# Kernel optimization log

Measured on AMD Instinct MI355X. Metric: run time of the kernel, lower is better.

Reference implementation:

```python
import jax, jax.numpy as jnp
import numpy as np

B, T, D = 2, 1024, 1024
H, HKV = 16, 8
HD = D // H           # 64
NREP = H // HKV       # 2
NLAYERS = 3
MAXKV = T * NLAYERS   # 3072
EPS = 1e-5


def setup_inputs() -> dict:
    key = jax.random.key(0)
    ks = jax.random.split(key, 8)
    # rotary tables over full accumulated-KV range
    inv_freq = 1.0 / (10000.0 ** (jnp.arange(0, HD, 2, dtype=jnp.float32) / HD))  # (HD/2,)
    t = jnp.arange(MAXKV, dtype=jnp.float32)
    freqs = jnp.outer(t, inv_freq)  # (MAXKV, HD/2)
    return {
        "x": jax.random.normal(ks[0], (B, T, D), jnp.float32),
        "cos": jnp.cos(freqs),
        "sin": jnp.sin(freqs),
        "q_w": jax.random.normal(ks[1], (NLAYERS, D, D), jnp.float32) * 0.02,
        "k_w": jax.random.normal(ks[2], (NLAYERS, D // NREP, D), jnp.float32) * 0.02,
        "v_w": jax.random.normal(ks[3], (NLAYERS, D // NREP, D), jnp.float32) * 0.02,
        "ln_w": jnp.ones((NLAYERS, D), jnp.float32),
        "lam": jax.random.normal(ks[4], (NLAYERS,), jnp.float32) * 0.1,
        "out_w": jax.random.normal(ks[5], (D, D), jnp.float32) * 0.02,
        "final_ln_w": jnp.ones((D,), jnp.float32),
        "alpha": jnp.ones((1,), jnp.float32),
    }


def rmsnorm(x, w):
    return x * jax.lax.rsqrt(jnp.mean(x * x, axis=-1, keepdims=True) + EPS) * w


def rope(x, cos, sin):
    # x: (B, L, h, HD); cos/sin: (MAXKV, HD/2); flash_attn non-interleaved rotary
    L = x.shape[1]
    c = jnp.concatenate([cos[:L], cos[:L]], axis=-1)[None, :, None, :]
    s = jnp.concatenate([sin[:L], sin[:L]], axis=-1)[None, :, None, :]
    x1, x2 = jnp.split(x, 2, axis=-1)
    rot = jnp.concatenate([-x2, x1], axis=-1)
    return x * c + rot * s


def reference(x, cos, sin, q_w, k_w, v_w, ln_w, lam, out_w, final_ln_w, alpha):
    scale = HD ** -0.5
    # lambda weights: layernorm over sigmoid of the 3 scalars (biased var, eps=1e-5)
    s = jax.nn.sigmoid(lam)
    lw = (s - s.mean()) * jax.lax.rsqrt(s.var() + EPS)
    qidx = jnp.arange(T)
    k_list, v_list = [], []
    acc = jnp.zeros_like(x)
    for i in range(NLAYERS):
        q = (x @ q_w[i].T).reshape(B, T, H, HD)
        k = (x @ k_w[i].T).reshape(B, T, HKV, HD)
        v = (x @ v_w[i].T).reshape(B, T, HKV, HD)
        k_list.append(k)
        v_list.append(v)
        K = jnp.concatenate(k_list, axis=1)  # (B, L, HKV, HD), L=(i+1)*T
        V = jnp.concatenate(v_list, axis=1)
        L = K.shape[1]
        qr = rope(q, cos, sin)
        Kr = rope(K, cos, sin)  # whole buffer re-rotated each layer, as in original
        Kr = jnp.repeat(Kr, NREP, axis=2)  # GQA expand
        Vr = jnp.repeat(V, NREP, axis=2)
        scores = jnp.einsum('bqhd,bkhd->bhqk', qr, Kr) * scale
        # flash_attn causal=True with kv_len > q_len aligns bottom-right
        mask = jnp.arange(L)[None, :] <= (qidx + (L - T))[:, None]
        scores = jnp.where(mask[None, None], scores, -jnp.inf)
        attn = jax.nn.softmax(scores, axis=-1)
        o = jnp.einsum('bhqk,bkhd->bqhd', attn, Vr).reshape(B, T, D)
        acc = acc + rmsnorm(o, ln_w[i]) * lw[i]
    out = rmsnorm(acc + alpha * x, final_ln_w)
    return out @ out_w.T
```

## Files before the change

kernel.cpp:

```cpp
#include <hip/hip_runtime.h>
#include <type_traits>
#include <utility>

typedef unsigned short u16;
typedef unsigned int u32;
typedef short short8 __attribute__((ext_vector_type(8)));
typedef __bf16 bf16x8 __attribute__((ext_vector_type(8)));
typedef float floatx4 __attribute__((ext_vector_type(4)));

template <typename V, typename = void> struct MfmaTakes : std::false_type {};
template <typename V>
struct MfmaTakes<V, std::void_t<decltype(__builtin_amdgcn_mfma_f32_16x16x32_bf16(
    std::declval<V>(), std::declval<V>(), std::declval<floatx4>(), 0, 0, 0))>>
    : std::true_type {};

template <typename V>
__device__ __forceinline__ floatx4 mfma_impl(V a, V b, floatx4 c, std::true_type) {
  return __builtin_amdgcn_mfma_f32_16x16x32_bf16(a, b, c, 0, 0, 0);
}
template <typename V>
__device__ __forceinline__ floatx4 mfma_impl(V a, V b, floatx4 c, std::false_type) {
  return __builtin_amdgcn_mfma_f32_16x16x32_bf16(
      __builtin_bit_cast(bf16x8, a), __builtin_bit_cast(bf16x8, b), c, 0, 0, 0);
}
__device__ __forceinline__ floatx4 MFMA16(short8 a, short8 b, floatx4 c) {
  return mfma_impl<short8>(a, b, c, MfmaTakes<short8>{});
}

__device__ __forceinline__ u16 f2bf(float f) {
  union { float f; unsigned u; } x; x.f = f;
  unsigned r = (x.u + 0x7fffu + ((x.u >> 16) & 1u)) >> 16;
  return (u16)r;
}
__device__ __forceinline__ float bf2f(u16 v) {
  union { unsigned u; float f; } x; x.u = ((unsigned)v) << 16; return x.f;
}
__device__ __forceinline__ u32 packbf(float lo, float hi) {
  return (__float_as_uint(hi) & 0xffff0000u) | (__float_as_uint(lo) >> 16);
}
__device__ __forceinline__ u32 pack2bf(float lo, float hi) {
  return ((u32)f2bf(hi) << 16) | (u32)f2bf(lo);
}

#if defined(__has_builtin)
#if __has_builtin(__builtin_amdgcn_global_load_lds)
#define HAS_GLLDS 1
#endif
#endif
__device__ __forceinline__ void stage16(const u16* g, u16* lbase, int lane) {
#ifdef HAS_GLLDS
  __builtin_amdgcn_global_load_lds(
      (__attribute__((address_space(1))) void*)(g),
      (__attribute__((address_space(3))) void*)(lbase), 16, 0, 0);
#else
  *(uint4*)(lbase + lane * 8) = *(const uint4*)g;
#endif
}

__global__ __launch_bounds__(256) void prep_kernel(
    const float* __restrict__ x, const float* __restrict__ qw,
    const float* __restrict__ kw, const float* __restrict__ vw,
    const float* __restrict__ outw, const float* __restrict__ lam,
    u16* __restrict__ xb, u16* __restrict__ wcat, u16* __restrict__ outwb,
    float* __restrict__ lwbuf) {
  size_t gid = (size_t)blockIdx.x * 256 + threadIdx.x;
  if (gid == 0) {
    float s0 = 1.f / (1.f + expf(-lam[0]));
    float s1 = 1.f / (1.f + expf(-lam[1]));
    float s2 = 1.f / (1.f + expf(-lam[2]));
    float mean = (s0 + s1 + s2) * (1.f / 3.f);
    float d0 = s0 - mean, d1 = s1 - mean, d2 = s2 - mean;
    float var = (d0 * d0 + d1 * d1 + d2 * d2) * (1.f / 3.f);
    float r = rsqrtf(var + 1e-5f);
    lwbuf[0] = d0 * r; lwbuf[1] = d1 * r; lwbuf[2] = d2 * r;
  }
  if (gid < 524288) {
    float4 v = ((const float4*)x)[gid];
    ushort4 o; o.x = f2bf(v.x); o.y = f2bf(v.y); o.z = f2bf(v.z); o.w = f2bf(v.w);
    ((ushort4*)xb)[gid] = o;
    return;
  }
  size_t g2 = gid - 524288;
  if (g2 < 1572864) {
    int col4 = (int)(g2 & 255);
    int n = (int)(g2 >> 8);
    int layer = n >> 11, r = n & 2047;
    const float* srcrow;
    if (r < 1024) srcrow = qw + ((size_t)(layer * 1024 + r) << 10);
    else if (r < 1536) srcrow = kw + ((size_t)(layer * 512 + (r - 1024)) << 10);
    else srcrow = vw + ((size_t)(layer * 512 + (r - 1536)) << 10);
    float4 v = ((const float4*)srcrow)[col4];
    ushort4 o; o.x = f2bf(v.x); o.y = f2bf(v.y); o.z = f2bf(v.z); o.w = f2bf(v.w);
    ((ushort4*)wcat)[g2] = o;
    return;
  }
  size_t g3 = g2 - 1572864;
  if (g3 < 262144) {
    float4 v = ((const float4*)outw)[g3];
    ushort4 o; o.x = f2bf(v.x); o.y = f2bf(v.y); o.z = f2bf(v.z); o.w = f2bf(v.w);
    ((ushort4*)outwb)[g3] = o;
  }
}

__global__ __launch_bounds__(256) void gemm_qkv(
    const u16* __restrict__ A, const u16* __restrict__ Bw,
    const float* __restrict__ cosb, const float* __restrict__ sinb,
    u16* __restrict__ qr, u16* __restrict__ kr, u16* __restrict__ vt) {
  __shared__ u16 As[128][64];
  __shared__ u16 Bs[128][64];
  const unsigned flat = blockIdx.x;
  const int bm = (flat >> 3) & 15;
  const int bn = ((flat >> 7) << 3) + (flat & 7);
  const int tid = threadIdx.x;
  const int wave = tid >> 6, lane = tid & 63;
  const int quad = lane >> 4, l16 = lane & 15;
  const int wm = wave & 1, wn = wave >> 1;
  const int srow = lane >> 3, skc = (lane & 7) * 8;
  floatx4 acc[4][4];
#pragma unroll
  for (int i = 0; i < 4; i++)
#pragma unroll
    for (int j = 0; j < 4; j++) { acc[i][j][0] = 0.f; acc[i][j][1] = 0.f; acc[i][j][2] = 0.f; acc[i][j][3] = 0.f; }
  const u16* Abase = A + (size_t)(bm * 128) * 1024;
  const u16* Bbase = Bw + (size_t)(bn * 128) * 1024;
  for (int k0 = 0; k0 < 1024; k0 += 64) {
    __syncthreads();
#pragma unroll
    for (int i = 0; i < 4; i++) {
      int ch = wave * 4 + i;
      stage16(Abase + (size_t)(ch * 8 + srow) * 1024 + k0 + skc, &As[ch * 8][0], lane);
      stage16(Bbase + (size_t)(ch * 8 + srow) * 1024 + k0 + skc, &Bs[ch * 8][0], lane);
    }
    __syncthreads();
#pragma unroll
    for (int kf = 0; kf < 2; kf++) {
      short8 af[4], bf[4];
#pragma unroll
      for (int mi = 0; mi < 4; mi++)
        af[mi] = *(const short8*)(&As[wm * 64 + mi * 16 + l16][kf * 32 + quad * 8]);
#pragma unroll
      for (int ni = 0; ni < 4; ni++)
        bf[ni] = *(const short8*)(&Bs[wn * 64 + ni * 16 + l16][kf * 32 + quad * 8]);
#pragma unroll
      for (int mi = 0; mi < 4; mi++)
#pragma unroll
        for (int ni = 0; ni < 4; ni++)
          acc[mi][ni] = MFMA16(af[mi], bf[ni], acc[mi][ni]);
    }
  }
  const int f0 = bn * 128 + wn * 64;
  const int lay = f0 >> 11;
  const int r0 = f0 & 2047;
  const int mrow0 = bm * 128 + wm * 64;
  if (r0 < 1024) {
    const int h = r0 >> 6;
#pragma unroll
    for (int mi = 0; mi < 4; mi++)
#pragma unroll
      for (int rr = 0; rr < 4; rr++) {
        int m = mrow0 + mi * 16 + quad * 4 + rr;
        int b = m >> 10, t = m & 1023;
        const float* cp = cosb + (size_t)t * 32;
        const float* sp = sinb + (size_t)t * 32;
        float c0 = cp[l16], s0 = sp[l16];
        float c1 = cp[16 + l16], s1 = sp[16 + l16];
        float x10 = acc[mi][0][rr], x20 = acc[mi][2][rr];
        float x11 = acc[mi][1][rr], x21 = acc[mi][3][rr];
        u16* row = qr + ((((size_t)lay * 2 + b) * 16 + h) * 1024 + t) * 64;
        row[l16]      = f2bf((x10 * c0 - x20 * s0) * 0.125f);
        row[16 + l16] = f2bf((x11 * c1 - x21 * s1) * 0.125f);
        row[32 + l16] = f2bf((x20 * c0 + x10 * s0) * 0.125f);
        row[48 + l16] = f2bf((x21 * c1 + x11 * s1) * 0.125f);
      }
  } else if (r0 < 1536) {
    const int hk = (r0 - 1024) >> 6;
#pragma unroll
    for (int mi = 0; mi < 4; mi++)
#pragma unroll
      for (int rr = 0; rr < 4; rr++) {
        int m = mrow0 + mi * 16 + quad * 4 + rr;
        int b = m >> 10, t = m & 1023;
        int pos = lay * 1024 + t;
        const float* cp = cosb + (size_t)pos * 32;
        const float* sp = sinb + (size_t)pos * 32;
        float c0 = cp[l16], s0 = sp[l16];
        float c1 = cp[16 + l16], s1 = sp[16 + l16];
        float x10 = acc[mi][0][rr], x20 = acc[mi][2][rr];
        float x11 = acc[mi][1][rr], x21 = acc[mi][3][rr];
        u16* row = kr + (((size_t)(b * 8 + hk)) * 3072 + pos) * 64;
        row[l16]      = f2bf(x10 * c0 - x20 * s0);
        row[16 + l16] = f2bf(x11 * c1 - x21 * s1);
        row[32 + l16] = f2bf(x20 * c0 + x10 * s0);
        row[48 + l16] = f2bf(x21 * c1 + x11 * s1);
      }
  } else {
    const int hv = (r0 - 1536) >> 6;
#pragma unroll
    for (int mi = 0; mi < 4; mi++) {
      int m0 = mrow0 + mi * 16 + quad * 4;
      int b = m0 >> 10;
      int pos0 = lay * 1024 + (m0 & 1023);
      u16* colbase = vt + ((size_t)(b * 8 + hv) * 64) * 3072 + pos0;
#pragma unroll
      for (int ni = 0; ni < 4; ni++) {
        int d = ni * 16 + l16;
        uint2 st;
        st.x = pack2bf(acc[mi][ni][0], acc[mi][ni][1]);
        st.y = pack2bf(acc[mi][ni][2], acc[mi][ni][3]);
        *(uint2*)(colbase + (size_t)d * 3072) = st;
      }
    }
  }
}

__global__ __launch_bounds__(256) void gemm_bt(
    const u16* __restrict__ A, const u16* __restrict__ Bw,
    float* __restrict__ C, int N, int K) {
  __shared__ u16 As[64][72];
  __shared__ u16 Bs[64][72];
  const int bm = blockIdx.x, bn = blockIdx.y;
  const int tid = threadIdx.x;
  const int wave = tid >> 6, lane = tid & 63;
  const int quad = lane >> 4, l16 = lane & 15;
  const int lr = tid >> 2, lc = (tid & 3) << 4;
  floatx4 acc[4];
#pragma unroll
  for (int i = 0; i < 4; i++) { acc[i][0] = 0.f; acc[i][1] = 0.f; acc[i][2] = 0.f; acc[i][3] = 0.f; }
  const u16* Arow = A + (size_t)(bm * 64 + lr) * K;
  const u16* Brow = Bw + (size_t)(bn * 64 + lr) * K;
  for (int k0 = 0; k0 < K; k0 += 64) {
    __syncthreads();
    *(uint4*)(&As[lr][lc])     = *(const uint4*)(Arow + k0 + lc);
    *(uint4*)(&As[lr][lc + 8]) = *(const uint4*)(Arow + k0 + lc + 8);
    *(uint4*)(&Bs[lr][lc])     = *(const uint4*)(Brow + k0 + lc);
    *(uint4*)(&Bs[lr][lc + 8]) = *(const uint4*)(Brow + k0 + lc + 8);
    __syncthreads();
    const int mrow = wave * 16 + l16;
    short8 a0 = *(const short8*)(&As[mrow][quad * 8]);
    short8 a1 = *(const short8*)(&As[mrow][32 + quad * 8]);
#pragma unroll
    for (int ns = 0; ns < 4; ns++) {
      short8 b0 = *(const short8*)(&Bs[ns * 16 + l16][quad * 8]);
      short8 b1 = *(const short8*)(&Bs[ns * 16 + l16][32 + quad * 8]);
      acc[ns] = MFMA16(a0, b0, acc[ns]);
      acc[ns] = MFMA16(a1, b1, acc[ns]);
    }
  }
#pragma unroll
  for (int ns = 0; ns < 4; ns++)
#pragma unroll
    for (int r = 0; r < 4; r++) {
      int row = bm * 64 + wave * 16 + quad * 4 + r;
      int col = bn * 64 + ns * 16 + l16;
      C[(size_t)row * N + col] = acc[ns][r];
    }
}

__global__ __launch_bounds__(256) void attn_v5(
    const u16* __restrict__ qr, const u16* __restrict__ kr,
    const u16* __restrict__ vt, u16* __restrict__ obS,
    float* __restrict__ lbufp) {
  __shared__ u16 Kt[32][72];
  __shared__ u16 Vtt[64][40];
  __shared__ u16 Pw[4][16][40];
  const unsigned flat = blockIdx.x;
  const int bhz = (int)((flat >> 6) * 8 + (flat & 7));
  const int qtile = 7 - (int)((flat >> 3) & 7);
  const int z = bhz >> 5;
  const int bh = bhz & 31;
  const int lay = (z == 5) ? 0 : ((z == 0 || z == 4) ? 1 : 2);
  const int n = lay * 32 + qtile * 4 + 4;
  int kt0, kt1;
  if (lay == 0) { kt0 = 0; kt1 = n; }
  else if (lay == 1) { int hf = n >> 1; kt0 = (z == 0) ? 0 : hf; kt1 = (z == 0) ? hf : n; }
  else {
    int t1 = n / 3, t2 = (2 * n) / 3;
    kt0 = (z == 1) ? 0 : ((z == 2) ? t1 : t2);
    kt1 = (z == 1) ? t1 : ((z == 2) ? t2 : n);
  }
  const int maskkt = lay * 32 + qtile * 4;
  const int b = bh >> 4, h = bh & 15, hk = h >> 1;
  const int tid = threadIdx.x, wave = tid >> 6, lane = tid & 63;
  const int quad = lane >> 4, l16 = lane & 15;
  const int qeffbase = lay * 1024 + qtile * 128 + wave * 32;
  const u16* qpb = qr + ((((size_t)lay * 2 + b) * 16 + h) * 1024
                         + qtile * 128 + wave * 32 + l16) * 64 + quad * 8;
  short8 qf[2][2];
  qf[0][0] = *(const short8*)(qpb);
  qf[0][1] = *(const short8*)(qpb + 32);
  qf[1][0] = *(const short8*)(qpb + 1024);
  qf[1][1] = *(const short8*)(qpb + 1056);
  const short8 ones = {16256, 16256, 16256, 16256, 16256, 16256, 16256, 16256};
  floatx4 oacc[2][4];
#pragma unroll
  for (int nt = 0; nt < 2; nt++)
#pragma unroll
    for (int dt = 0; dt < 4; dt++) { oacc[nt][dt][0] = 0.f; oacc[nt][dt][1] = 0.f; oacc[nt][dt][2] = 0.f; oacc[nt][dt][3] = 0.f; }
  floatx4 lacc[2];
  lacc[0][0] = 0.f; lacc[0][1] = 0.f; lacc[0][2] = 0.f; lacc[0][3] = 0.f;
  lacc[1] = lacc[0];
  const int ksr = tid >> 3, ksc = (tid & 7) * 8;
  const int vdr = tid >> 2, vdc = (tid & 3) * 8;
  const u16* kp = kr + ((size_t)(b * 8 + hk) * 3072 + kt0 * 32 + ksr) * 64 + ksc;
  const u16* vp = vt + ((size_t)(b * 8 + hk) * 64 + vdr) * 3072 + kt0 * 32 + vdc;
  uint4 kA = *(const uint4*)kp;
  uint4 vA = *(const uint4*)vp;
  for (int kt = kt0; kt < kt1; kt++) {
    kp += 2048; vp += 32;
    __syncthreads();
    *(uint4*)(&Kt[ksr][ksc])  = kA;
    *(uint4*)(&Vtt[vdr][vdc]) = vA;
    if (kt + 1 < kt1) { kA = *(const uint4*)kp; vA = *(const uint4*)vp; }
    __syncthreads();
    const bool needmask = (kt >= maskkt);
    uint2 pk[2][2];
#pragma unroll
    for (int mt = 0; mt < 2; mt++) {
      short8 kfa = *(const short8*)(&Kt[mt * 16 + l16][quad * 8]);
      short8 kfb = *(const short8*)(&Kt[mt * 16 + l16][32 + quad * 8]);
      const int keyb = kt * 32 + mt * 16 + quad * 4;
#pragma unroll
      for (int nt = 0; nt < 2; nt++) {
        floatx4 s; s[0] = 0.f; s[1] = 0.f; s[2] = 0.f; s[3] = 0.f;
        s = MFMA16(kfa, qf[nt][0], s);
        s = MFMA16(kfb, qf[nt][1], s);
        float p0 = __expf(s[0]), p1 = __expf(s[1]);
        float p2 = __expf(s[2]), p3 = __expf(s[3]);
        if (needmask) {
          int qpos = qeffbase + nt * 16 + l16;
          if (keyb + 0 > qpos) p0 = 0.f;
          if (keyb + 1 > qpos) p1 = 0.f;
          if (keyb + 2 > qpos) p2 = 0.f;
          if (keyb + 3 > qpos) p3 = 0.f;
        }
        pk[mt][nt].x = packbf(p0, p1);
        pk[mt][nt].y = packbf(p2, p3);
      }
    }
    short8 vf[4];
#pragma unroll
    for (int dt = 0; dt < 4; dt++)
      vf[dt] = *(const short8*)(&Vtt[dt * 16 + l16][quad * 8]);
#pragma unroll
    for (int nt = 0; nt < 2; nt++) {
      *(uint2*)(&Pw[wave][l16][quad * 4])      = pk[0][nt];
      *(uint2*)(&Pw[wave][l16][16 + quad * 4]) = pk[1][nt];
      short8 pf = *(const short8*)(&Pw[wave][l16][quad * 8]);
      lacc[nt] = MFMA16(ones, pf, lacc[nt]);
#pragma unroll
      for (int dt = 0; dt < 4; dt++)
        oacc[nt][dt] = MFMA16(vf[dt], pf, oacc[nt][dt]);
    }
  }
  float* Pf = (float*)(&Pw[wave][0][0]);
  const int tt = lane >> 2, dd = (lane & 3) << 2;
#pragma unroll
  for (int nt = 0; nt < 2; nt++) {
    int t = qtile * 128 + wave * 32 + nt * 16 + l16;
    if (quad == 0)
      lbufp[((size_t)z * 2048 + b * 1024 + t) * 16 + h] = lacc[nt][0];
    int t2 = qtile * 128 + wave * 32 + nt * 16 + tt;
    u16* orow = obS + ((size_t)(z * 2 + b) * 1024 + t2) * 1024 + h * 64 + dd;
#pragma unroll
    for (int dt = 0; dt < 4; dt++) {
      *(floatx4*)(&Pf[l16 * 20 + quad * 4]) = oacc[nt][dt];
      floatx4 val = *(const floatx4*)(&Pf[tt * 20 + dd]);
      uint2 st; st.x = pack2bf(val[0], val[1]); st.y = pack2bf(val[2], val[3]);
      *(uint2*)(orow + dt * 16) = st;
    }
  }
}

__device__ __forceinline__ float block_sum(float v, float* red) {
  v += __shfl_xor(v, 32); v += __shfl_xor(v, 16); v += __shfl_xor(v, 8);
  v += __shfl_xor(v, 4);  v += __shfl_xor(v, 2);  v += __shfl_xor(v, 1);
  __syncthreads();
  if ((threadIdx.x & 63) == 0) red[threadIdx.x >> 6] = v;
  __syncthreads();
  return red[0] + red[1] + red[2] + red[3];
}

__global__ __launch_bounds__(256) void fused_norm(
    const u16* __restrict__ obS, const float* __restrict__ lbufp,
    const float* __restrict__ x, const float* __restrict__ lnw,
    const float* __restrict__ lwbuf, const float* __restrict__ flnw,
    const float* __restrict__ alphap, u16* __restrict__ y) {
  __shared__ float red[4];
  const int row = blockIdx.x, tid = threadIdx.x;
  float a[4] = {0.f, 0.f, 0.f, 0.f};
  const int nsl[3] = {1, 2, 3};
  const int sl[3][3] = {{5, 0, 0}, {0, 4, 0}, {1, 2, 3}};
#pragma unroll
  for (int l = 0; l < 3; l++) {
    float o0 = 0.f, o1 = 0.f, o2 = 0.f, o3 = 0.f, ls = 0.f;
#pragma unroll
    for (int si = 0; si < 3; si++) {
      if (si >= nsl[l]) break;
      int z = sl[l][si];
      uint2 v = ((const uint2*)(obS + ((size_t)z * 2048 + row) * 1024))[tid];
      o0 += bf2f((u16)(v.x & 0xffff)); o1 += bf2f((u16)(v.x >> 16));
      o2 += bf2f((u16)(v.y & 0xffff)); o3 += bf2f((u16)(v.y >> 16));
      ls += lbufp[((size_t)z * 2048 + row) * 16 + (tid >> 4)];
    }
    float linv = 1.f / ls;
    float v0 = o0 * linv, v1 = o1 * linv, v2 = o2 * linv, v3 = o3 * linv;
    float ss = v0 * v0 + v1 * v1 + v2 * v2 + v3 * v3;
    ss = block_sum(ss, red);
    float rstd = rsqrtf(ss * (1.f / 1024.f) + 1e-5f);
    float lw = lwbuf[l];
    float4 w = ((const float4*)(lnw + (size_t)l * 1024))[tid];
    a[0] += v0 * rstd * w.x * lw;
    a[1] += v1 * rstd * w.y * lw;
    a[2] += v2 * rstd * w.z * lw;
    a[3] += v3 * rstd * w.w * lw;
  }
  const float aa = alphap[0];
  float4 xv = ((const float4*)(x + (size_t)row * 1024))[tid];
  float v0 = a[0] + aa * xv.x, v1 = a[1] + aa * xv.y;
  float v2 = a[2] + aa * xv.z, v3 = a[3] + aa * xv.w;
  float ss = v0 * v0 + v1 * v1 + v2 * v2 + v3 * v3;
  ss = block_sum(ss, red);
  float rstd = rsqrtf(ss * (1.f / 1024.f) + 1e-5f);
  float4 fw = ((const float4*)flnw)[tid];
  ushort4 o;
  o.x = f2bf(v0 * rstd * fw.x); o.y = f2bf(v1 * rstd * fw.y);
  o.z = f2bf(v2 * rstd * fw.z); o.w = f2bf(v3 * rstd * fw.w);
  ((ushort4*)(y + (size_t)row * 1024))[tid] = o;
}

extern "C" void kernel_launch(void* const* d_in, const int* in_sizes, int n_in,
                              void* d_out, int out_size, void* d_ws, size_t ws_size,
                              hipStream_t stream) {
  const float* x     = (const float*)d_in[0];
  const float* cosb  = (const float*)d_in[1];
  const float* sinb  = (const float*)d_in[2];
  const float* qw    = (const float*)d_in[3];
  const float* kw    = (const float*)d_in[4];
  const float* vw    = (const float*)d_in[5];
  const float* lnw   = (const float*)d_in[6];
  const float* lam   = (const float*)d_in[7];
  const float* outw  = (const float*)d_in[8];
  const float* flnw  = (const float*)d_in[9];
  const float* alphap= (const float*)d_in[10];
  float* out = (float*)d_out;
  char* ws = (char*)d_ws;
  u16*   xb    = (u16*)  (ws + 0);
  u16*   wcat  = (u16*)  (ws + 4194304);
  u16*   obS   = (u16*)  (ws + 0);
  u16*   outwb = (u16*)  (ws + 25165824);
  float* lwbuf = (float*)(ws + 27262976);
  u16*   qr    = (u16*)  (ws + 27264000);
  u16*   kr    = (u16*)  (ws + 39846912);
  u16*   vt    = (u16*)  (ws + 46138368);
  float* lbufp = (float*)(ws + 52429824);
  u16*   yb    = (u16*)  (ws + 53216256);

  prep_kernel<<<9216, 256, 0, stream>>>(x, qw, kw, vw, outw, lam, xb, wcat, outwb, lwbuf);
  gemm_qkv<<<768, 256, 0, stream>>>(xb, wcat, cosb, sinb, qr, kr, vt);
  attn_v5<<<1536, 256, 0, stream>>>(qr, kr, vt, obS, lbufp);
  fused_norm<<<2048, 256, 0, stream>>>(obS, lbufp, x, lnw, lwbuf, flnw, alphap, yb);
  gemm_bt<<<dim3(32, 16), 256, 0, stream>>>(yb, outwb, out, 1024, 1024);
}
```

Before: 252.0 us.

## Stage QKV epilogue through LDS for coalesced stores; load V fragments directly

The QKV GEMM epilogue now writes rotated Q/K and transposed V tiles into a per-wave LDS scratch area (reusing As) and then emits 16-byte coalesced global stores, replacing scattered 2-byte and 8-byte writes. The attention kernel drops the shared V tile and instead has each lane load its MFMA V fragments straight from global memory, software-pipelined one key tile ahead. This removes LDS traffic and shared-memory footprint for V, but each wave now fetches V redundantly and keeps more registers live.

```diff
diff --git a/kernel.cpp b/kernel.cpp
--- a/kernel.cpp
+++ b/kernel.cpp
@@ -148,66 +148,69 @@
           acc[mi][ni] = MFMA16(af[mi], bf[ni], acc[mi][ni]);
     }
   }
+  __syncthreads();
+  u16* Tw = (&As[0][0]) + (unsigned)wave * 1056;
   const int f0 = bn * 128 + wn * 64;
   const int lay = f0 >> 11;
   const int r0 = f0 & 2047;
   const int mrow0 = bm * 128 + wm * 64;
-  if (r0 < 1024) {
-    const int h = r0 >> 6;
-#pragma unroll
-    for (int mi = 0; mi < 4; mi++)
+  const int jrd = lane & 7, trd = lane >> 3;
+  if (r0 < 1536) {
+    const bool isQ = (r0 < 1024);
+    const int h = isQ ? (r0 >> 6) : ((r0 - 1024) >> 6);
+    const float qscale = isQ ? 0.125f : 1.f;
+    const int posoff = isQ ? 0 : lay * 1024;
+#pragma unroll
+    for (int mi = 0; mi < 4; mi++) {
 #pragma unroll
       for (int rr = 0; rr < 4; rr++) {
         int m = mrow0 + mi * 16 + quad * 4 + rr;
-        int b = m >> 10, t = m & 1023;
-        const float* cp = cosb + (size_t)t * 32;
-        const float* sp = sinb + (size_t)t * 32;
-        float c0 = cp[l16], s0 = sp[l16];
-        float c1 = cp[16 + l16], s1 = sp[16 + l16];
-        float x10 = acc[mi][0][rr], x20 = acc[mi][2][rr];
-        float x11 = acc[mi][1][rr], x21 = acc[mi][3][rr];
-        u16* row = qr + ((((size_t)lay * 2 + b) * 16 + h) * 1024 + t) * 64;
-        row[l16]      = f2bf((x10 * c0 - x20 * s0) * 0.125f);
-        row[16 + l16] = f2bf((x11 * c1 - x21 * s1) * 0.125f);
-        row[32 + l16] = f2bf((x20 * c0 + x10 * s0) * 0.125f);
-        row[48 + l16] = f2bf((x21 * c1 + x11 * s1) * 0.125f);
-      }
-  } else if (r0 < 1536) {
-    const int hk = (r0 - 1024) >> 6;
-#pragma unroll
-    for (int mi = 0; mi < 4; mi++)
-#pragma unroll
-      for (int rr = 0; rr < 4; rr++) {
-        int m = mrow0 + mi * 16 + quad * 4 + rr;
-        int b = m >> 10, t = m & 1023;
-        int pos = lay * 1024 + t;
+        int t = m & 1023;
+        int pos = posoff + t;
         const float* cp = cosb + (size_t)pos * 32;
         const float* sp = sinb + (size_t)pos * 32;
         float c0 = cp[l16], s0 = sp[l16];
         float c1 = cp[16 + l16], s1 = sp[16 + l16];
         float x10 = acc[mi][0][rr], x20 = acc[mi][2][rr];
         float x11 = acc[mi][1][rr], x21 = acc[mi][3][rr];
-        u16* row = kr + (((size_t)(b * 8 + hk)) * 3072 + pos) * 64;
-        row[l16]      = f2bf(x10 * c0 - x20 * s0);
-        row[16 + l16] = f2bf(x11 * c1 - x21 * s1);
-        row[32 + l16] = f2bf(x20 * c0 + x10 * s0);
-        row[48 + l16] = f2bf(x21 * c1 + x11 * s1);
+        u16* trow = Tw + (quad * 4 + rr) * 66;
+        trow[l16]      = f2bf((x10 * c0 - x20 * s0) * qscale);
+        trow[16 + l16] = f2bf((x11 * c1 - x21 * s1) * qscale);
+        trow[32 + l16] = f2bf((x20 * c0 + x10 * s0) * qscale);
+        trow[48 + l16] = f2bf((x21 * c1 + x11 * s1) * qscale);
       }
+#pragma unroll
+      for (int half = 0; half < 2; half++) {
+        int tloc = trd + half * 8;
+        uint4 val = *(const uint4*)(Tw + tloc * 66 + jrd * 8);
+        int m = mrow0 + mi * 16 + tloc;
+        int b = m >> 10, t = m & 1023;
+        u16* dst;
+        if (isQ) dst = qr + ((((size_t)lay * 2 + b) * 16 + h) * 1024 + t) * 64;
+        else     dst = kr + (((size_t)(b * 8 + h)) * 3072 + lay * 1024 + t) * 64;
+        *(uint4*)(dst + jrd * 8) = val;
+      }
+    }
   } else {
     const int hv = (r0 - 1536) >> 6;
-#pragma unroll
-    for (int mi = 0; mi < 4; mi++) {
-      int m0 = mrow0 + mi * 16 + quad * 4;
-      int b = m0 >> 10;
-      int pos0 = lay * 1024 + (m0 & 1023);
-      u16* colbase = vt + ((size_t)(b * 8 + hv) * 64) * 3072 + pos0;
-#pragma unroll
-      for (int ni = 0; ni < 4; ni++) {
-        int d = ni * 16 + l16;
-        uint2 st;
-        st.x = pack2bf(acc[mi][ni][0], acc[mi][ni][1]);
-        st.y = pack2bf(acc[mi][ni][2], acc[mi][ni][3]);
-        *(uint2*)(colbase + (size_t)d * 3072) = st;
+    const int b = mrow0 >> 10;
+    const int posb = lay * 1024 + (mrow0 & 1023);
+#pragma unroll
+    for (int ni = 0; ni < 4; ni++) {
+#pragma unroll
+      for (int mi = 0; mi < 4; mi++) {
+        u16* trow = Tw + l16 * 66 + mi * 16 + quad * 4;
+        trow[0] = f2bf(acc[mi][ni][0]);
+        trow[1] = f2bf(acc[mi][ni][1]);
+        trow[2] = f2bf(acc[mi][ni][2]);
+        trow[3] = f2bf(acc[mi][ni][3]);
+      }
+#pragma unroll
+      for (int half = 0; half < 2; half++) {
+        int dloc = trd + half * 8;
+        uint4 val = *(const uint4*)(Tw + dloc * 66 + jrd * 8);
+        u16* dst = vt + ((size_t)(b * 8 + hv) * 64 + ni * 16 + dloc) * 3072 + posb + jrd * 8;
+        *(uint4*)dst = val;
       }
     }
   }
@@ -256,12 +259,11 @@
     }
 }
 
-__global__ __launch_bounds__(256) void attn_v5(
+__global__ __launch_bounds__(256) void attn_v6(
     const u16* __restrict__ qr, const u16* __restrict__ kr,
     const u16* __restrict__ vt, u16* __restrict__ obS,
     float* __restrict__ lbufp) {
   __shared__ u16 Kt[32][72];
-  __shared__ u16 Vtt[64][40];
   __shared__ u16 Pw[4][16][40];
   const unsigned flat = blockIdx.x;
   const int bhz = (int)((flat >> 6) * 8 + (flat & 7));
@@ -300,17 +302,25 @@
   lacc[0][0] = 0.f; lacc[0][1] = 0.f; lacc[0][2] = 0.f; lacc[0][3] = 0.f;
   lacc[1] = lacc[0];
   const int ksr = tid >> 3, ksc = (tid & 7) * 8;
-  const int vdr = tid >> 2, vdc = (tid & 3) * 8;
   const u16* kp = kr + ((size_t)(b * 8 + hk) * 3072 + kt0 * 32 + ksr) * 64 + ksc;
-  const u16* vp = vt + ((size_t)(b * 8 + hk) * 64 + vdr) * 3072 + kt0 * 32 + vdc;
+  const u16* vwb = vt + (size_t)(b * 8 + hk) * 64 * 3072 + (size_t)l16 * 3072 + quad * 8;
   uint4 kA = *(const uint4*)kp;
-  uint4 vA = *(const uint4*)vp;
+  short8 vf[4], vfN[4];
+#pragma unroll
+  for (int dt = 0; dt < 4; dt++)
+    vfN[dt] = *(const short8*)(vwb + (size_t)(dt * 16) * 3072 + kt0 * 32);
   for (int kt = kt0; kt < kt1; kt++) {
-    kp += 2048; vp += 32;
-    __syncthreads();
-    *(uint4*)(&Kt[ksr][ksc])  = kA;
-    *(uint4*)(&Vtt[vdr][vdc]) = vA;
-    if (kt + 1 < kt1) { kA = *(const uint4*)kp; vA = *(const uint4*)vp; }
+    kp += 2048;
+    __syncthreads();
+    *(uint4*)(&Kt[ksr][ksc]) = kA;
+    if (kt + 1 < kt1) kA = *(const uint4*)kp;
+#pragma unroll
+    for (int dt = 0; dt < 4; dt++) vf[dt] = vfN[dt];
+    if (kt + 1 < kt1) {
+#pragma unroll
+      for (int dt = 0; dt < 4; dt++)
+        vfN[dt] = *(const short8*)(vwb + (size_t)(dt * 16) * 3072 + (kt + 1) * 32);
+    }
     __syncthreads();
     const bool needmask = (kt >= maskkt);
     uint2 pk[2][2];
@@ -337,10 +347,6 @@
         pk[mt][nt].y = packbf(p2, p3);
       }
     }
-    short8 vf[4];
-#pragma unroll
-    for (int dt = 0; dt < 4; dt++)
-      vf[dt] = *(const short8*)(&Vtt[dt * 16 + l16][quad * 8]);
 #pragma unroll
     for (int nt = 0; nt < 2; nt++) {
       *(uint2*)(&Pw[wave][l16][quad * 4])      = pk[0][nt];
@@ -457,7 +463,7 @@
 
   prep_kernel<<<9216, 256, 0, stream>>>(x, qw, kw, vw, outw, lam, xb, wcat, outwb, lwbuf);
   gemm_qkv<<<768, 256, 0, stream>>>(xb, wcat, cosb, sinb, qr, kr, vt);
-  attn_v5<<<1536, 256, 0, stream>>>(qr, kr, vt, obS, lbufp);
+  attn_v6<<<1536, 256, 0, stream>>>(qr, kr, vt, obS, lbufp);
   fused_norm<<<2048, 256, 0, stream>>>(obS, lbufp, x, lnw, lwbuf, flnw, alphap, yb);
   gemm_bt<<<dim3(32, 16), 256, 0, stream>>>(yb, outwb, out, 1024, 1024);
 }
```

After: 282.0 us. 11.9% more time.

## Process two KV tiles per barrier pair and reorder attention blocks by schedule table

Applied to the files above, without the earlier changes.

The attention loop now stages two 32-key K/V tiles into double LDS buffers per synchronisation round and prefetches the next two tiles into registers, halving the number of __syncthreads per key range. Block-to-work mapping is replaced by a constant schedule table that orders (split, qtile) pairs so heavy work items launch first, while the 32 batch-heads are grouped contiguously. This aims to cut barrier overhead and improve load balance, at the cost of more LDS and registers, which may lower occupancy.

```diff
diff --git a/kernel.cpp b/kernel.cpp
--- a/kernel.cpp
+++ b/kernel.cpp
@@ -56,6 +56,23 @@
   *(uint4*)(lbase + lane * 8) = *(const uint4*)g;
 #endif
 }
+
+__constant__ unsigned char SCHED48[48] = {
+  47, 7, 39, 15, 23, 31,
+  22, 30,
+   6, 38, 14, 29,
+  13, 21,
+   5, 37, 12, 20, 28, 46,
+  19, 27,
+   4, 36, 11, 26,
+  10, 18,
+   3, 35,  9, 17, 25, 45,
+  16, 24,
+   2, 34,  8,
+   1, 33, 44,
+   0, 32,
+  43, 42, 41, 40
+};
 
 __global__ __launch_bounds__(256) void prep_kernel(
     const float* __restrict__ x, const float* __restrict__ qw,
@@ -256,18 +273,16 @@
     }
 }
 
-__global__ __launch_bounds__(256) void attn_v5(
+__global__ __launch_bounds__(256) void attn_v9(
     const u16* __restrict__ qr, const u16* __restrict__ kr,
     const u16* __restrict__ vt, u16* __restrict__ obS,
     float* __restrict__ lbufp) {
-  __shared__ u16 Kt[32][72];
-  __shared__ u16 Vtt[64][40];
+  __shared__ u16 Kt[2][32][72];
+  __shared__ u16 Vtt[2][64][40];
   __shared__ u16 Pw[4][16][40];
-  const unsigned flat = blockIdx.x;
-  const int bhz = (int)((flat >> 6) * 8 + (flat & 7));
-  const int qtile = 7 - (int)((flat >> 3) & 7);
-  const int z = bhz >> 5;
-  const int bh = bhz & 31;
+  const int pair = SCHED48[blockIdx.x >> 5];
+  const int z = pair >> 3, qtile = pair & 7;
+  const int bh = blockIdx.x & 31;
   const int lay = (z == 5) ? 0 : ((z == 0 || z == 4) ? 1 : 2);
   const int n = lay * 32 + qtile * 4 + 4;
   int kt0, kt1;
@@ -286,10 +301,11 @@
   const u16* qpb = qr + ((((size_t)lay * 2 + b) * 16 + h) * 1024
                          + qtile * 128 + wave * 32 + l16) * 64 + quad * 8;
   short8 qf[2][2];
-  qf[0][0] = *(const short8*)(qpb);
-  qf[0][1] = *(const short8*)(qpb + 32);
-  qf[1][0] = *(const short8*)(qpb + 1024);
-  qf[1][1] = *(const short8*)(qpb + 1056);
+#pragma unroll
+  for (int nt = 0; nt < 2; nt++) {
+    qf[nt][0] = *(const short8*)(qpb + nt * 1024);
+    qf[nt][1] = *(const short8*)(qpb + nt * 1024 + 32);
+  }
   const short8 ones = {16256, 16256, 16256, 16256, 16256, 16256, 16256, 16256};
   floatx4 oacc[2][4];
 #pragma unroll
@@ -303,22 +319,14 @@
   const int vdr = tid >> 2, vdc = (tid & 3) * 8;
   const u16* kp = kr + ((size_t)(b * 8 + hk) * 3072 + kt0 * 32 + ksr) * 64 + ksc;
   const u16* vp = vt + ((size_t)(b * 8 + hk) * 64 + vdr) * 3072 + kt0 * 32 + vdc;
-  uint4 kA = *(const uint4*)kp;
-  uint4 vA = *(const uint4*)vp;
-  for (int kt = kt0; kt < kt1; kt++) {
-    kp += 2048; vp += 32;
-    __syncthreads();
-    *(uint4*)(&Kt[ksr][ksc])  = kA;
-    *(uint4*)(&Vtt[vdr][vdc]) = vA;
-    if (kt + 1 < kt1) { kA = *(const uint4*)kp; vA = *(const uint4*)vp; }
-    __syncthreads();
-    const bool needmask = (kt >= maskkt);
+  auto process = [&](int bi, int ktc) {
+    const bool needmask = (ktc >= maskkt);
     uint2 pk[2][2];
 #pragma unroll
     for (int mt = 0; mt < 2; mt++) {
-      short8 kfa = *(const short8*)(&Kt[mt * 16 + l16][quad * 8]);
-      short8 kfb = *(const short8*)(&Kt[mt * 16 + l16][32 + quad * 8]);
-      const int keyb = kt * 32 + mt * 16 + quad * 4;
+      short8 kfa = *(const short8*)(&Kt[bi][mt * 16 + l16][quad * 8]);
+      short8 kfb = *(const short8*)(&Kt[bi][mt * 16 + l16][32 + quad * 8]);
+      const int keyb = ktc * 32 + mt * 16 + quad * 4;
 #pragma unroll
       for (int nt = 0; nt < 2; nt++) {
         floatx4 s; s[0] = 0.f; s[1] = 0.f; s[2] = 0.f; s[3] = 0.f;
@@ -340,7 +348,7 @@
     short8 vf[4];
 #pragma unroll
     for (int dt = 0; dt < 4; dt++)
-      vf[dt] = *(const short8*)(&Vtt[dt * 16 + l16][quad * 8]);
+      vf[dt] = *(const short8*)(&Vtt[bi][dt * 16 + l16][quad * 8]);
 #pragma unroll
     for (int nt = 0; nt < 2; nt++) {
       *(uint2*)(&Pw[wave][l16][quad * 4])      = pk[0][nt];
@@ -351,6 +359,29 @@
       for (int dt = 0; dt < 4; dt++)
         oacc[nt][dt] = MFMA16(vf[dt], pf, oacc[nt][dt]);
     }
+  };
+  uint4 kg[2], vg[2];
+  kg[0] = *(const uint4*)kp; vg[0] = *(const uint4*)vp;
+  if (kt1 - kt0 > 1) { kg[1] = *(const uint4*)(kp + 2048); vg[1] = *(const uint4*)(vp + 32); }
+  kp += 4096; vp += 64;
+  int kt = kt0;
+  while (kt < kt1) {
+    const int np = (kt1 - kt >= 2) ? 2 : 1;
+    __syncthreads();
+    *(uint4*)(&Kt[0][ksr][ksc])  = kg[0];
+    *(uint4*)(&Vtt[0][vdr][vdc]) = vg[0];
+    if (np == 2) {
+      *(uint4*)(&Kt[1][ksr][ksc])  = kg[1];
+      *(uint4*)(&Vtt[1][vdr][vdc]) = vg[1];
+    }
+    const int rem = kt1 - (kt + np);
+    if (rem > 0) { kg[0] = *(const uint4*)kp; vg[0] = *(const uint4*)vp; }
+    if (rem > 1) { kg[1] = *(const uint4*)(kp + 2048); vg[1] = *(const uint4*)(vp + 32); }
+    kp += 4096; vp += 64;
+    __syncthreads();
+    process(0, kt);
+    if (np == 2) process(1, kt + 1);
+    kt += np;
   }
   float* Pf = (float*)(&Pw[wave][0][0]);
   const int tt = lane >> 2, dd = (lane & 3) << 2;
@@ -457,7 +488,7 @@
 
   prep_kernel<<<9216, 256, 0, stream>>>(x, qw, kw, vw, outw, lam, xb, wcat, outwb, lwbuf);
   gemm_qkv<<<768, 256, 0, stream>>>(xb, wcat, cosb, sinb, qr, kr, vt);
-  attn_v5<<<1536, 256, 0, stream>>>(qr, kr, vt, obS, lbufp);
+  attn_v9<<<1536, 256, 0, stream>>>(qr, kr, vt, obS, lbufp);
   fused_norm<<<2048, 256, 0, stream>>>(obS, lbufp, x, lnw, lwbuf, flnw, alphap, yb);
   gemm_bt<<<dim3(32, 16), 256, 0, stream>>>(yb, outwb, out, 1024, 1024);
 }
```

Result: slower. 286.4 us (+13.6%).
